# Optimization experiments

Measured on AMD Instinct MI355X. Metric: run time of the kernel, lower is better.

Reference implementation:

```python
import jax, jax.numpy as jnp
import numpy as np
from jax import lax

BACKEND_IN = [512, 512, 512, 512, 256, 128]
BACKEND_OUT = [512, 512, 512, 256, 128, 64]
BN_EPS = 1e-5


def setup_inputs() -> dict:
    key = jax.random.key(0)
    ks = jax.random.split(key, 20)
    B, H, W = 8, 64, 64
    inp = {}
    inp['x'] = jax.random.normal(ks[0], (B, 512, H, W), jnp.float32)
    inp['y'] = jax.random.normal(ks[1], (B, 512), jnp.float32)
    inp['fc_w'] = jax.random.normal(ks[2], (6, 100, 512), jnp.float32) * 0.02
    inp['fc_b'] = jnp.zeros((6, 100), jnp.float32)
    for i in range(6):
        inp[f'wb{i}'] = jax.random.normal(ks[3 + i], (BACKEND_OUT[i] * 3, 100), jnp.float32) * 0.01
        inp[f'wc{i}'] = jax.random.normal(ks[9 + i], (BACKEND_IN[i] * 3, 100), jnp.float32) * 0.01
    inp['out_w'] = jax.random.normal(ks[15], (1, 64, 1, 1), jnp.float32) * 0.01
    inp['out_b'] = jnp.zeros((1,), jnp.float32)
    return inp


def _forward(x, y, fc_w, fc_b, wbs, wcs, out_w, out_b):
    B = x.shape[0]
    for i in range(6):
        # hypernetwork: Linear(512 -> 100)
        wa = y @ fc_w[i].T + fc_b[i]                    # (B, 100)
        # diag_embed + WB/WC matmul chain collapses to a 3-way contraction:
        # w[b,o,i] = sum_k WB[o,k] * wa[b,k] * WC[i,k]
        w = jnp.einsum('ok,bk,ik->boi', wbs[i], wa, wcs[i])  # (B, 3*cout, 3*cin)
        cout = wbs[i].shape[0] // 3
        cin = wcs[i].shape[0] // 3
        w = w.reshape(B, cout, cin, 3, 3)               # same row-major view as torch
        H, W = x.shape[2], x.shape[3]
        # per-sample dynamic conv == one grouped conv with groups = B
        xg = x.reshape(1, B * cin, H, W)
        wg = w.reshape(B * cout, cin, 3, 3)
        o = lax.conv_general_dilated(
            xg, wg, window_strides=(1, 1), padding=((2, 2), (2, 2)),
            rhs_dilation=(2, 2), feature_group_count=B,
            dimension_numbers=('NCHW', 'OIHW', 'NCHW'))
        x = o.reshape(B, cout, H, W)
        # BatchNorm2d (training mode, gamma=1, beta=0) + ReLU
        mean = x.mean(axis=(0, 2, 3), keepdims=True)
        var = ((x - mean) ** 2).mean(axis=(0, 2, 3), keepdims=True)
        x = jax.nn.relu((x - mean) * lax.rsqrt(var + BN_EPS))
    # 1x1 output conv (64 -> 1)
    out = jnp.einsum('bchw,oc->bohw', x, out_w[:, :, 0, 0]) + out_b.reshape(1, -1, 1, 1)
    # F.upsample(scale_factor=8), default nearest
    out = jnp.repeat(jnp.repeat(out, 8, axis=2), 8, axis=3)
    return out


def reference(x, y, fc_w, fc_b, wb0, wb1, wb2, wb3, wb4, wb5,
              wc0, wc1, wc2, wc3, wc4, wc5, out_w, out_b):
    wbs = [wb0, wb1, wb2, wb3, wb4, wb5]
    wcs = [wc0, wc1, wc2, wc3, wc4, wc5]
    return _forward(x, y, fc_w, fc_b, wbs, wcs, out_w, out_b)
```

## Files before the change

kernel.cpp:

```cpp
#include <hip/hip_runtime.h>
#include <stdint.h>

typedef __attribute__((ext_vector_type(8))) short short8;
typedef __attribute__((ext_vector_type(4))) float f32x4;
typedef __attribute__((ext_vector_type(4))) unsigned int u32x4;

struct Ptr6 { const float* p[6]; };

struct LTab {
  const unsigned short* wbh; const unsigned short* wach;
  unsigned short* wboi; unsigned short* w2;
  int cumg[7]; int cumt[7];
  int mblk[6]; int nblk[6]; int M3[6]; int N3[6]; int CINt[6]; int COUTt[6];
  long moff[6]; long coff[6]; long woff[6];
};

__device__ __forceinline__ float bf2f(unsigned short u){
  union { unsigned int i; float f; } x; x.i = ((unsigned int)u) << 16; return x.f;
}
__device__ __forceinline__ unsigned short f2bf(float f){
  union { float f; unsigned int i; } x; x.f = f;
  unsigned int r = x.i + 0x7fffu + ((x.i >> 16) & 1u);
  return (unsigned short)(r >> 16);
}

__global__ void wa_kernel(const float* __restrict__ y, const float* __restrict__ fcw,
                          const float* __restrict__ fcb, float* __restrict__ wa){
  int l = blockIdx.x >> 3, b = blockIdx.x & 7;
  int k = threadIdx.x;
  if (k >= 100) return;
  const float* yr = y + b*512;
  const float* wr = fcw + (l*100 + k)*512;
  float s = 0.f;
  for (int j=0;j<512;j++) s += yr[j]*wr[j];
  wa[(l*8+b)*100 + k] = s + fcb[l*100 + k];
}

__global__ void wbh_all_kernel(Ptr6 wb, unsigned short* __restrict__ o){
  const int roff1=1536, roff2=3072, roff3=4608, roff4=5376, roff5=5760;
  int idx = blockIdx.x*256 + threadIdx.x;
  int row = idx >> 7, k = idx & 127;
  int l, r;
  if      (row < roff1){ l=0; r=row; }
  else if (row < roff2){ l=1; r=row-roff1; }
  else if (row < roff3){ l=2; r=row-roff2; }
  else if (row < roff4){ l=3; r=row-roff3; }
  else if (row < roff5){ l=4; r=row-roff4; }
  else                 { l=5; r=row-roff5; }
  const int m3[6] = {1536,1536,1536,768,384,192};
  float v = (r < m3[l] && k < 100) ? wb.p[l][r*100 + k] : 0.f;
  o[idx] = f2bf(v);
}

__global__ void wach_all_kernel(Ptr6 wc, const float* __restrict__ wa,
                                unsigned short* __restrict__ o){
  const int c1=12288, c2=24576, c3=36864, c4=49152, c5=55296;
  int idx = blockIdx.x*256 + threadIdx.x;
  int row = idx >> 7, k = idx & 127;
  int l, r, n3;
  if      (row < c1){ l=0; r=row;    n3=1536; }
  else if (row < c2){ l=1; r=row-c1; n3=1536; }
  else if (row < c3){ l=2; r=row-c2; n3=1536; }
  else if (row < c4){ l=3; r=row-c3; n3=1536; }
  else if (row < c5){ l=4; r=row-c4; n3=768; }
  else              { l=5; r=row-c5; n3=384; }
  int b = r / n3, i = r % n3;
  float v = (k < 100) ? wa[(l*8+b)*100 + k] * wc.p[l][i*100 + k] : 0.f;
  o[idx] = f2bf(v);
}

__device__ __forceinline__ void wgen_body(
    const unsigned short* __restrict__ wbh, const unsigned short* __restrict__ wach,
    unsigned short* __restrict__ wboi, int M3, int N3, int m0, int n0, int b,
    unsigned short* At, unsigned short* Bt){
  const int t = threadIdx.x;
  const unsigned short* As = wbh + (size_t)m0*128;
  const unsigned short* Bs = wach + ((size_t)b*N3 + n0)*128;
  #pragma unroll
  for (int j=0;j<8;j++){
    int c = j*256 + t;
    int row = c >> 4, q = c & 15;
    *(u32x4*)&At[row*136 + q*8] = *(const u32x4*)&As[row*128 + q*8];
    *(u32x4*)&Bt[row*136 + q*8] = *(const u32x4*)&Bs[row*128 + q*8];
  }
  __syncthreads();
  const int wv = t >> 6, lane = t & 63;
  const int wm = (wv >> 1)*64, wn = (wv & 1)*64;
  const int lr = lane & 15, lkg = lane >> 4, lk8 = lkg*8;
  f32x4 acc[4][4];
  #pragma unroll
  for (int i=0;i<4;i++) for (int j=0;j<4;j++) acc[i][j] = (f32x4){0,0,0,0};
  #pragma unroll
  for (int kc=0;kc<4;kc++){
    short8 a[4], bv[4];
    #pragma unroll
    for (int mi=0;mi<4;mi++) a[mi] = *(const short8*)&At[(wm+mi*16+lr)*136 + kc*32 + lk8];
    #pragma unroll
    for (int ni=0;ni<4;ni++) bv[ni] = *(const short8*)&Bt[(wn+ni*16+lr)*136 + kc*32 + lk8];
    #pragma unroll
    for (int mi=0;mi<4;mi++)
      #pragma unroll
      for (int ni=0;ni<4;ni++)
        acc[mi][ni] = __builtin_amdgcn_mfma_f32_16x16x32_bf16(a[mi], bv[ni], acc[mi][ni], 0,0,0);
  }
  #pragma unroll
  for (int mi=0;mi<4;mi++)
    #pragma unroll
    for (int ni=0;ni<4;ni++)
      #pragma unroll
      for (int r=0;r<4;r++){
        int o = m0 + wm + mi*16 + lkg*4 + r;
        int i = n0 + wn + ni*16 + lr;
        if (o < M3) wboi[((size_t)b*M3 + o)*N3 + i] = f2bf(acc[mi][ni][r]);
      }
}

__global__ __launch_bounds__(256) void wgen_all_kernel(LTab tab){
  __shared__ unsigned short At[128*136];
  __shared__ unsigned short Bt[128*136];
  int bid = blockIdx.x;
  int l = 0;
  #pragma unroll
  for (int i=1;i<6;i++) if (bid >= tab.cumg[i]) l = i;
  int rem = bid - tab.cumg[l];
  int mb = rem % tab.mblk[l];
  int r2 = rem / tab.mblk[l];
  int nb = r2 % tab.nblk[l];
  int b  = r2 / tab.nblk[l];
  wgen_body(tab.wbh + tab.moff[l]*128, tab.wach + tab.coff[l]*128,
            tab.wboi + tab.woff[l], tab.M3[l], tab.N3[l], mb*128, nb*128, b, At, Bt);
}

__global__ __launch_bounds__(256) void wgen_kernel(
    const unsigned short* __restrict__ wbh, const unsigned short* __restrict__ wach,
    unsigned short* __restrict__ wboi, int M3, int N3){
  __shared__ unsigned short At[128*136];
  __shared__ unsigned short Bt[128*136];
  wgen_body(wbh, wach, wboi, M3, N3, blockIdx.x*128, blockIdx.y*128, blockIdx.z, At, Bt);
}

__device__ __forceinline__ void wtr_body(
    const unsigned short* __restrict__ wboi, unsigned short* __restrict__ W2,
    int CIN, int COUT, int co, int b, unsigned short* buf){
  const int t = threadIdx.x;
  const int n = 9*CIN;
  const unsigned short* src = wboi + ((size_t)b*3*COUT + 3*co)*(size_t)(3*CIN);
  for (int i = t*8; i < n; i += 2048) *(u32x4*)&buf[i] = *(const u32x4*)&src[i];
  __syncthreads();
  const int nch = n >> 3;
  const int cpr = CIN >> 3;
  for (int idx = t; idx < nch; idx += 256){
    int tap = idx / cpr, cig = idx - tap*cpr;
    short8 v;
    #pragma unroll
    for (int j=0;j<8;j++) v[j] = (short)buf[(cig*8+j)*9 + tap];
    *(short8*)&W2[(((size_t)(b*9 + tap)*COUT) + co)*CIN + cig*8] = v;
  }
}

__global__ void wtr_all_kernel(LTab tab){
  __shared__ unsigned short buf[9*512];
  int bid = blockIdx.x;
  int l = 0;
  #pragma unroll
  for (int i=1;i<6;i++) if (bid >= tab.cumt[i]) l = i;
  int rem = bid - tab.cumt[l];
  int co = rem % tab.COUTt[l];
  int b  = rem / tab.COUTt[l];
  wtr_body(tab.wboi + tab.woff[l], tab.w2 + tab.woff[l], tab.CINt[l], tab.COUTt[l], co, b, buf);
}

__global__ void wtr_kernel(const unsigned short* __restrict__ wboi, unsigned short* __restrict__ W2,
                           int CIN, int COUT){
  __shared__ unsigned short buf[9*512];
  wtr_body(wboi, W2, CIN, COUT, blockIdx.x % COUT, blockIdx.x / COUT, buf);
}

__global__ void castx_kernel(const float* __restrict__ x, unsigned short* __restrict__ act){
  __shared__ float tile[64][65];
  int bid = blockIdx.x;
  int ct = bid & 7; int hp = (bid >> 3) % 68; int b = bid / 544;
  int c0 = ct * 64;
  int t = threadIdx.x;
  unsigned short* orow = act + ((size_t)(b*68 + hp)*68)*512;
  if (hp < 2 || hp >= 66){
    for (int idx = t; idx < 68*64; idx += 256){
      int wp = idx >> 6, c = idx & 63;
      orow[wp*512 + c0 + c] = 0;
    }
    return;
  }
  int h = hp - 2;
  for (int idx = t; idx < 64*64; idx += 256){
    int r = idx >> 6, w = idx & 63;
    tile[r][w] = x[((size_t)(b*512 + c0 + r)*64 + h)*64 + w];
  }
  __syncthreads();
  for (int idx = t; idx < 68*64; idx += 256){
    int wp = idx >> 6, c = idx & 63;
    float v = (wp < 2 || wp >= 66) ? 0.f : tile[c][wp-2];
    orow[wp*512 + c0 + c] = f2bf(v);
  }
}

template<int CIN, int COUT>
__global__ __launch_bounds__(256, 2) void conv_kernel(
    const unsigned short* __restrict__ act, const unsigned short* __restrict__ W2,
    float* __restrict__ cbuf, float* __restrict__ partial){
  __shared__ unsigned short Al[9*256*8];
  __shared__ unsigned short Pl[20*20*4*8];
  const int co0 = blockIdx.x * 64;
  const int h0 = (blockIdx.y >> 2) * 16;
  const int w0 = (blockIdx.y & 3) * 16;
  const int b = blockIdx.z;
  const int t = threadIdx.x;
  const int wv = t >> 6, lane = t & 63;
  const int lr = lane & 15, lkg = lane >> 4;

  const unsigned short* actb = act + (size_t)b*68*68*CIN;
  const unsigned short* wb = W2 + (size_t)b*9*COUT*CIN;

  f32x4 acc[4][4];
  #pragma unroll
  for (int i=0;i<4;i++) for (int j=0;j<4;j++) acc[i][j] = (f32x4){0,0,0,0};

  for (int cs = 0; cs < CIN/32; ++cs){
    const int cb = cs*32;
    #pragma unroll
    for (int j=0;j<9;j++){
      int c = j*256 + t;
      int tap = c >> 8, rem = c & 255;
      int co = rem >> 2, q = rem & 3;
      u32x4 v = *(const u32x4*)&wb[((size_t)(tap*COUT + co0 + co))*CIN + cb + q*8];
      *(u32x4*)&Al[(tap*256 + q*64 + (co^q))*8] = v;
    }
    #pragma unroll
    for (int j=0;j<7;j++){
      int c = j*256 + t;
      if (c < 1600){
        int ph = c/80, rem = c%80, pw = rem>>2, q = rem&3;
        u32x4 v = *(const u32x4*)&actb[(size_t)((h0+ph)*68 + (w0+pw))*CIN + cb + q*8];
        *(u32x4*)&Pl[((ph*20+pw)*4 + (q ^ ((pw>>1)&3)))*8] = v;
      }
    }
    __syncthreads();
    #pragma unroll
    for (int kh=0;kh<3;kh++){
      #pragma unroll
      for (int kw=0;kw<3;kw++){
        const int tap = kh*3 + kw;
        short8 a[4], bv[4];
        #pragma unroll
        for (int mi=0;mi<4;mi++)
          a[mi] = *(const short8*)&Al[(tap*256 + lkg*64 + ((mi*16+lr)^lkg))*8];
        #pragma unroll
        for (int ni=0;ni<4;ni++){
          int pr = wv*4 + ni + 2*kh;
          int pc = lr + 2*kw;
          bv[ni] = *(const short8*)&Pl[((pr*20+pc)*4 + (lkg ^ ((pc>>1)&3)))*8];
        }
        #pragma unroll
        for (int mi=0;mi<4;mi++)
          #pragma unroll
          for (int ni=0;ni<4;ni++)
            acc[mi][ni] = __builtin_amdgcn_mfma_f32_16x16x32_bf16(a[mi], bv[ni], acc[mi][ni], 0,0,0);
      }
    }
    __syncthreads();
  }
  float* ob = cbuf + (size_t)b*64*64*COUT;
  #pragma unroll
  for (int mi=0;mi<4;mi++){
    int co = co0 + mi*16 + lkg*4;
    #pragma unroll
    for (int ni=0;ni<4;ni++){
      int hh = h0 + wv*4 + ni;
      int ww = w0 + lr;
      *(f32x4*)&ob[(size_t)(hh*64 + ww)*COUT + co] = acc[mi][ni];
    }
  }
  float ps[4][4], pq[4][4];
  #pragma unroll
  for (int mi=0;mi<4;mi++)
    #pragma unroll
    for (int r=0;r<4;r++){ ps[mi][r]=0.f; pq[mi][r]=0.f; }
  #pragma unroll
  for (int mi=0;mi<4;mi++)
    #pragma unroll
    for (int ni=0;ni<4;ni++)
      #pragma unroll
      for (int r=0;r<4;r++){
        float v = acc[mi][ni][r];
        ps[mi][r] += v; pq[mi][r] += v*v;
      }
  #pragma unroll
  for (int m=1;m<16;m<<=1)
    #pragma unroll
    for (int mi=0;mi<4;mi++)
      #pragma unroll
      for (int r=0;r<4;r++){
        ps[mi][r] += __shfl_xor(ps[mi][r], m);
        pq[mi][r] += __shfl_xor(pq[mi][r], m);
      }
  if (lr == 0){
    const int tile = (blockIdx.y*8 + blockIdx.z)*4 + wv;
    #pragma unroll
    for (int mi=0;mi<4;mi++)
      #pragma unroll
      for (int r=0;r<4;r++){
        int co = co0 + mi*16 + lkg*4 + r;
        ((float2*)partial)[co*512 + tile] = make_float2(ps[mi][r], pq[mi][r]);
      }
  }
}

__global__ void bnfin_kernel(const float* __restrict__ partial, float* __restrict__ bnmr, int C){
  int c = blockIdx.x*256 + threadIdx.x;
  if (c >= C) return;
  float s=0.f, q=0.f;
  for (int tl=0; tl<512; ++tl){
    float2 v = ((const float2*)partial)[c*512 + tl];
    s += v.x; q += v.y;
  }
  const float inv_n = 1.f/32768.f;
  float mean = s*inv_n;
  float var = q*inv_n - mean*mean;
  bnmr[c] = mean;
  bnmr[512 + c] = rsqrtf(var + 1e-5f);
}

__global__ void bnapply_kernel(const float* __restrict__ cbuf, const float* __restrict__ bnmr,
                               unsigned short* __restrict__ actout, int lc){
  const int C = 1 << lc;
  const int bid = blockIdx.x;
  const int hp = bid % 68, b = bid / 68;
  const int t = threadIdx.x;
  unsigned short* orow = actout + (((size_t)(b*68 + hp))*68 << lc);
  const bool hb = (hp < 2) || (hp >= 66);
  const int n = 68 << lc;
  for (int idx = t; idx < n; idx += 256){
    int wp = idx >> lc, c = idx & (C-1);
    float v = 0.f;
    if (!hb && wp >= 2 && wp < 66){
      float xx = cbuf[((((size_t)b*64 + (hp-2))*64 + (wp-2)) << lc) + c];
      float z = (xx - bnmr[c]) * bnmr[512 + c];
      v = z > 0.f ? z : 0.f;
    }
    orow[idx] = f2bf(v);
  }
}

__global__ void convup_kernel(const unsigned short* __restrict__ act, const float* __restrict__ ow,
                              const float* __restrict__ ob, float* __restrict__ out){
  int idx = blockIdx.x*256 + threadIdx.x;
  int b = idx >> 12, p = idx & 4095;
  int h = p >> 6, w = p & 63;
  const unsigned short* ar = act + (((size_t)(b*68 + h+2))*68 + (w+2))*64;
  float s = 0.f;
  #pragma unroll
  for (int c=0;c<64;c++) s += bf2f(ar[c]) * ow[c];
  s += ob[0];
  f32x4 v = {s,s,s,s};
  float* o = out + (((size_t)b*512 + h*8)*512) + w*8;
  #pragma unroll
  for (int rr=0;rr<8;rr++){
    *(f32x4*)(o + (size_t)rr*512) = v;
    *(f32x4*)(o + (size_t)rr*512 + 4) = v;
  }
}

extern "C" void kernel_launch(void* const* d_in, const int* in_sizes, int n_in,
                              void* d_out, int out_size, void* d_ws, size_t ws_size,
                              hipStream_t stream){
  const float* x   = (const float*)d_in[0];
  const float* y   = (const float*)d_in[1];
  const float* fcw = (const float*)d_in[2];
  const float* fcb = (const float*)d_in[3];
  Ptr6 wbp, wcp;
  bool dictOrder = (in_sizes[10] == 76800);
  for (int i=0;i<6;i++){
    if (dictOrder){ wbp.p[i] = (const float*)d_in[4+2*i]; wcp.p[i] = (const float*)d_in[5+2*i]; }
    else          { wbp.p[i] = (const float*)d_in[4+i];   wcp.p[i] = (const float*)d_in[10+i]; }
  }
  const float* ow  = (const float*)d_in[16];
  const float* obp = (const float*)d_in[17];
  float* out = (float*)d_out;

  static const int CIN[6]  = {512,512,512,512,256,128};
  static const int COUT[6] = {512,512,512,256,128,64};
  static const int MPAD[6] = {1536,1536,1536,768,384,256};
  static const int LC[6]   = {9,9,9,8,7,6};
  static const long MOFF[6] = {0,1536,3072,4608,5376,5760};
  static const long COFF[6] = {0,12288,24576,36864,49152,55296};
  static const long WOFF[6] = {0,18874368,37748736,56623104,66060288,68419584};

  const size_t actBytes  = (size_t)8*68*68*512*2;
  const size_t cbufBytes = (size_t)8*64*64*512*4;
  const size_t wAllBytes = (size_t)69009408*2;
  const size_t w2OneBytes= (size_t)18874368*2;
  const size_t partBytes = (size_t)512*512*2*4;

  char* ws = (char*)d_ws; size_t off = 0;
  auto alloc = [&](size_t bytes)->void*{ void* p = ws + off; off += (bytes + 255) & ~(size_t)255; return p; };

  size_t needBatched = 0;
  {
    size_t o2 = 0;
    auto a2 = [&](size_t b){ o2 += (b + 255) & ~(size_t)255; };
    a2(actBytes); a2(actBytes); a2(cbufBytes); a2(wAllBytes);
    a2(6*8*100*4); a2((size_t)6016*128*2); a2((size_t)58368*128*2); a2(partBytes); a2(1024*4);
    needBatched = o2;
  }
  const bool batched = (ws_size >= needBatched);

  unsigned short* actA = (unsigned short*)alloc(actBytes);
  unsigned short* actB = (unsigned short*)alloc(actBytes);
  float* cbuf = (float*)alloc(cbufBytes);
  unsigned short* W2all = nullptr; unsigned short* W2one = nullptr; unsigned short* wboi = nullptr;
  if (batched){
    W2all = (unsigned short*)alloc(wAllBytes);
    wboi  = (unsigned short*)ws;
  } else {
    W2one = (unsigned short*)alloc(w2OneBytes);
    wboi  = (unsigned short*)cbuf;
  }
  float* wa = (float*)alloc(6*8*100*4);
  unsigned short* wbh = (unsigned short*)alloc((size_t)6016*128*2);
  unsigned short* wach = (unsigned short*)alloc((size_t)58368*128*2);
  float* partial = (float*)alloc(partBytes);
  float* bnmr = (float*)alloc(1024*4);

  wa_kernel<<<48, 128, 0, stream>>>(y, fcw, fcb, wa);
  wbh_all_kernel<<<6016*128/256, 256, 0, stream>>>(wbp, wbh);
  wach_all_kernel<<<58368*128/256, 256, 0, stream>>>(wcp, wa, wach);

  if (batched){
    LTab tab;
    tab.wbh = wbh; tab.wach = wach; tab.wboi = wboi; tab.w2 = W2all;
    int gsz[6], tsz[6];
    for (int l=0;l<6;l++){
      tab.mblk[l] = MPAD[l]/128; tab.nblk[l] = 3*CIN[l]/128;
      tab.M3[l] = 3*COUT[l]; tab.N3[l] = 3*CIN[l];
      tab.CINt[l] = CIN[l]; tab.COUTt[l] = COUT[l];
      tab.moff[l] = MOFF[l]; tab.coff[l] = COFF[l]; tab.woff[l] = WOFF[l];
      gsz[l] = tab.mblk[l]*tab.nblk[l]*8; tsz[l] = 8*COUT[l];
    }
    tab.cumg[0] = 0; tab.cumt[0] = 0;
    for (int l=0;l<6;l++){ tab.cumg[l+1] = tab.cumg[l] + gsz[l]; tab.cumt[l+1] = tab.cumt[l] + tsz[l]; }
    wgen_all_kernel<<<tab.cumg[6], 256, 0, stream>>>(tab);
    wtr_all_kernel<<<tab.cumt[6], 256, 0, stream>>>(tab);
  }

  castx_kernel<<<8*68*8, 256, 0, stream>>>(x, actA);

  unsigned short* ain = actA; unsigned short* aout = actB;
  for (int l=0;l<6;l++){
    const unsigned short* W2l;
    if (batched){
      W2l = W2all + WOFF[l];
    } else {
      int M3 = 3*COUT[l], N3 = 3*CIN[l];
      wgen_kernel<<<dim3(MPAD[l]/128, N3/128, 8), 256, 0, stream>>>(
          wbh + (size_t)MOFF[l]*128, wach + (size_t)COFF[l]*128, wboi, M3, N3);
      wtr_kernel<<<8*COUT[l], 256, 0, stream>>>(wboi, W2one, CIN[l], COUT[l]);
      W2l = W2one;
    }
    switch(l){
      case 0: case 1: case 2:
        conv_kernel<512,512><<<dim3(8,16,8),256,0,stream>>>(ain, W2l, cbuf, partial); break;
      case 3:
        conv_kernel<512,256><<<dim3(4,16,8),256,0,stream>>>(ain, W2l, cbuf, partial); break;
      case 4:
        conv_kernel<256,128><<<dim3(2,16,8),256,0,stream>>>(ain, W2l, cbuf, partial); break;
      case 5:
        conv_kernel<128,64><<<dim3(1,16,8),256,0,stream>>>(ain, W2l, cbuf, partial); break;
    }
    bnfin_kernel<<<2, 256, 0, stream>>>(partial, bnmr, COUT[l]);
    bnapply_kernel<<<8*68, 256, 0, stream>>>(cbuf, bnmr, aout, LC[l]);
    unsigned short* tmp = ain; ain = aout; aout = tmp;
  }
  convup_kernel<<<(8*4096)/256, 256, 0, stream>>>(ain, ow, obp, out);
}
```

Before: 1.255 ms.

## Load conv tiles via direct global-to-LDS loads and parallelize BN stat reduction

The conv kernel's per-chunk staging of weight and padded activation tiles now uses global_load_lds 16-byte direct loads into shared memory. Per-lane source pointers are precomputed once and advanced each channel chunk, which removes the register round-trip and address math from the loop. The BN finalize kernel now assigns one 32-lane group per channel with a shuffle reduction, replacing a serial 512-step loop per thread spread over only two blocks. The direct-to-LDS path relies on the lane-to-LDS layout matching the existing swizzle and holds 16 pointers per thread, which may increase register pressure.

```diff
diff --git a/kernel.cpp b/kernel.cpp
--- a/kernel.cpp
+++ b/kernel.cpp
@@ -22,6 +22,11 @@
   union { float f; unsigned int i; } x; x.f = f;
   unsigned int r = x.i + 0x7fffu + ((x.i >> 16) & 1u);
   return (unsigned short)(r >> 16);
+}
+
+__device__ __forceinline__ void gll16(const void* g, void* l){
+  __builtin_amdgcn_global_load_lds((const __attribute__((address_space(1))) void*)g,
+                                   (__attribute__((address_space(3))) void*)l, 16, 0, 0);
 }
 
 __global__ void wa_kernel(const float* __restrict__ y, const float* __restrict__ fcw,
@@ -220,27 +225,37 @@
   const unsigned short* actb = act + (size_t)b*68*68*CIN;
   const unsigned short* wb = W2 + (size_t)b*9*COUT*CIN;
 
+  const unsigned short* ga[16];
+  #pragma unroll
+  for (int j=0;j<16;j++){
+    int id = wv*16 + j;
+    if (id < 36){
+      int tap = id >> 2, q = id & 3;
+      int co = lane ^ q;
+      ga[j] = &wb[((size_t)(tap*COUT + co0 + co))*CIN + q*8];
+    } else if (id < 61){
+      int s = (id-36)*64 + lane;
+      int pp = s >> 2;
+      int ph = pp/20, pw = pp - ph*20;
+      int q = (s&3) ^ ((pw>>1)&3);
+      ga[j] = &actb[(size_t)((h0+ph)*68 + (w0+pw))*CIN + q*8];
+    } else {
+      ga[j] = nullptr;
+    }
+  }
+
   f32x4 acc[4][4];
   #pragma unroll
   for (int i=0;i<4;i++) for (int j=0;j<4;j++) acc[i][j] = (f32x4){0,0,0,0};
 
   for (int cs = 0; cs < CIN/32; ++cs){
-    const int cb = cs*32;
-    #pragma unroll
-    for (int j=0;j<9;j++){
-      int c = j*256 + t;
-      int tap = c >> 8, rem = c & 255;
-      int co = rem >> 2, q = rem & 3;
-      u32x4 v = *(const u32x4*)&wb[((size_t)(tap*COUT + co0 + co))*CIN + cb + q*8];
-      *(u32x4*)&Al[(tap*256 + q*64 + (co^q))*8] = v;
-    }
-    #pragma unroll
-    for (int j=0;j<7;j++){
-      int c = j*256 + t;
-      if (c < 1600){
-        int ph = c/80, rem = c%80, pw = rem>>2, q = rem&3;
-        u32x4 v = *(const u32x4*)&actb[(size_t)((h0+ph)*68 + (w0+pw))*CIN + cb + q*8];
-        *(u32x4*)&Pl[((ph*20+pw)*4 + (q ^ ((pw>>1)&3)))*8] = v;
+    #pragma unroll
+    for (int j=0;j<16;j++){
+      int id = wv*16 + j;
+      if (id < 61){
+        unsigned short* lp = (id < 36) ? &Al[id*512] : &Pl[(id-36)*512];
+        gll16((const void*)ga[j], (void*)lp);
+        ga[j] += 32;
       }
     }
     __syncthreads();
@@ -315,18 +330,27 @@
 }
 
 __global__ void bnfin_kernel(const float* __restrict__ partial, float* __restrict__ bnmr, int C){
-  int c = blockIdx.x*256 + threadIdx.x;
+  int lane = threadIdx.x & 31, ch8 = threadIdx.x >> 5;
+  int c = blockIdx.x*8 + ch8;
   if (c >= C) return;
+  const float2* p = (const float2*)partial + (size_t)c*512;
   float s=0.f, q=0.f;
-  for (int tl=0; tl<512; ++tl){
-    float2 v = ((const float2*)partial)[c*512 + tl];
+  for (int tl=lane; tl<512; tl+=32){
+    float2 v = p[tl];
     s += v.x; q += v.y;
   }
-  const float inv_n = 1.f/32768.f;
-  float mean = s*inv_n;
-  float var = q*inv_n - mean*mean;
-  bnmr[c] = mean;
-  bnmr[512 + c] = rsqrtf(var + 1e-5f);
+  #pragma unroll
+  for (int m=1;m<32;m<<=1){
+    s += __shfl_xor(s, m);
+    q += __shfl_xor(q, m);
+  }
+  if (lane == 0){
+    const float inv_n = 1.f/32768.f;
+    float mean = s*inv_n;
+    float var = q*inv_n - mean*mean;
+    bnmr[c] = mean;
+    bnmr[512 + c] = rsqrtf(var + 1e-5f);
+  }
 }
 
 __global__ void bnapply_kernel(const float* __restrict__ cbuf, const float* __restrict__ bnmr,
@@ -475,7 +499,7 @@
       case 5:
         conv_kernel<128,64><<<dim3(1,16,8),256,0,stream>>>(ain, W2l, cbuf, partial); break;
     }
-    bnfin_kernel<<<2, 256, 0, stream>>>(partial, bnmr, COUT[l]);
+    bnfin_kernel<<<COUT[l]/8, 256, 0, stream>>>(partial, bnmr, COUT[l]);
     bnapply_kernel<<<8*68, 256, 0, stream>>>(cbuf, bnmr, aout, LC[l]);
     unsigned short* tmp = ain; ain = aout; aout = tmp;
   }
```

Result: faster. 1.169 ms (-6.9%).
